# Kernel optimization log

Hardware: AMD Instinct MI355X
Metric: run time of the kernel (lower is better)

The kernel has to match this reference:

```python
import jax, jax.numpy as jnp
import numpy as np

VOL = 100.0  # cubic volume (100,100,100)


def _forward(x, positions, input_weights, features, output_weights,
             connection_radii, thresholds, n_iterations):
    # clamp positions into the volume (per-axis, min 0.1, max VOL-0.1)
    pos = jnp.clip(positions, 0.1, VOL - 0.1)                      # [N,3]
    radii = jnp.clip(connection_radii, 1.0, 50.0)                  # [N]
    # pairwise Euclidean distances via ||a||^2 + ||b||^2 - 2ab (avoids [N,N,3])
    sq = jnp.sum(pos * pos, axis=1)
    d2 = jnp.maximum(sq[:, None] + sq[None, :] - 2.0 * (pos @ pos.T), 0.0)
    pos_mask = d2 > 0.0
    dist = jnp.where(pos_mask, jnp.sqrt(jnp.where(pos_mask, d2, 1.0)), 0.0)  # [N,N]
    max_r = jnp.max(radii)
    conn_mask = (dist < max_r).astype(dist.dtype)
    atten = jnp.exp(-jnp.minimum(dist / (radii[:, None] + 1e-6), 20.0)) * conn_mask
    # feature similarity (F.normalize uses eps as a clamp-min on the norm)
    fn = features / jnp.maximum(jnp.linalg.norm(features, axis=1, keepdims=True), 1e-6)
    feat_sim = fn @ fn.T                                            # [N,N]
    cw = atten * (0.3 + 0.7 * jnp.clip(feat_sim, -1.0, 1.0))
    cw = cw / (jnp.sum(cw, axis=1, keepdims=True) + 1e-6)           # row-normalized [N,N]
    # spatial input / output gating along x-axis
    xc = jnp.clip(pos[:, 0] / VOL, 0.0, 1.0)                        # [N]
    iw = jnp.exp(-3.0 * xc)
    iw = iw / (jnp.sum(iw) + 1e-6)
    act = (x @ input_weights.T) * iw                                # [B,N]
    for _ in range(n_iterations):
        act = jnp.minimum(jax.nn.relu(act + act @ cw.T - thresholds), 100.0)
    ow = jnp.exp(3.0 * (xc - 1.0))
    ow = ow / (jnp.sum(ow) + 1e-6)
    return (act * ow) @ output_weights                              # [B,out]


def setup_inputs() -> dict:
    key = jax.random.key(0)
    ks = jax.random.split(key, 5)
    N, IN, OUT, FD, B = 8000, 784, 10, 32, 64
    return {
        "x": jax.random.normal(ks[0], (B, IN), jnp.float32),
        "positions": jax.random.uniform(ks[1], (N, 3), jnp.float32) * VOL,
        "input_weights": jax.random.normal(ks[2], (N, IN), jnp.float32) * 0.01,
        "features": jax.random.normal(ks[3], (N, FD), jnp.float32) * 0.1,
        "output_weights": jax.random.normal(ks[4], (N, OUT), jnp.float32) * 0.01,
        "connection_radii": jnp.ones((N,), jnp.float32) * 15.0,
        "thresholds": jnp.zeros((N,), jnp.float32),
        "n_iterations": 2,
    }


def reference(x, positions, input_weights, features, output_weights,
              connection_radii, thresholds, n_iterations):
    return _forward(x, positions, input_weights, features, output_weights,
                    connection_radii, thresholds, n_iterations)
```

## Files before the change

kernel.cpp:

```cpp
#include <hip/hip_runtime.h>
#include <hip/hip_bf16.h>
#include <math.h>

#define VOLF 100.0f
#define FD 32
#define OUT_DIM 10
#define MAXN 320
#define MAX_LAUNCH_ITERS 4
#define SRW 2
#define SRB 8
#define OB 128
#define CHUNK 28
#define NCHUNK 7
#define LDP 68
#define PS 8

__global__ __launch_bounds__(256) void k_prext(
    const float* __restrict__ x, const float* __restrict__ positions,
    const float* __restrict__ radii_in, const float* __restrict__ features,
    float* __restrict__ xT, float* __restrict__ posx4,
    float* __restrict__ radii, float* __restrict__ e_iw, float* __restrict__ e_ow,
    float* __restrict__ fn, float* __restrict__ scal, int N, int B, int IN, int nxt)
{
    if ((int)blockIdx.x < nxt) {
        int idx = blockIdx.x * 256 + threadIdx.x;
        if (idx < B * IN) {
            int b = idx / IN, k = idx % IN;
            xT[(size_t)k * B + b] = x[idx];
        }
        return;
    }
    int i = (blockIdx.x - nxt) * 256 + threadIdx.x;
    float my_iw = 0.0f, my_ow = 0.0f, my_r = 0.0f;
    if (i < N) {
        float px = fminf(fmaxf(positions[3*i+0], 0.1f), VOLF - 0.1f);
        float py = fminf(fmaxf(positions[3*i+1], 0.1f), VOLF - 0.1f);
        float pz = fminf(fmaxf(positions[3*i+2], 0.1f), VOLF - 0.1f);
        float sq = px*px + py*py + pz*pz;
        posx4[4*i+0] = px; posx4[4*i+1] = py; posx4[4*i+2] = pz; posx4[4*i+3] = sq;
        float r = fminf(fmaxf(radii_in[i], 1.0f), 50.0f);
        radii[i] = r; my_r = r;
        float xc = fminf(fmaxf(px / VOLF, 0.0f), 1.0f);
        my_iw = expf(-3.0f * xc);
        my_ow = expf(3.0f * (xc - 1.0f));
        e_iw[i] = my_iw; e_ow[i] = my_ow;
        float s = 0.0f;
        #pragma unroll
        for (int k = 0; k < FD; k++) { float v = features[(size_t)i*FD + k]; s += v*v; }
        float nrm = fmaxf(sqrtf(s), 1e-6f);
        #pragma unroll
        for (int k = 0; k < FD; k++) fn[(size_t)i*FD + k] = features[(size_t)i*FD + k] / nrm;
    }
    __shared__ float red[256];
    red[threadIdx.x] = my_iw; __syncthreads();
    for (int s = 128; s > 0; s >>= 1) { if (threadIdx.x < s) red[threadIdx.x] += red[threadIdx.x + s]; __syncthreads(); }
    if (threadIdx.x == 0) atomicAdd(&scal[0], red[0]);
    __syncthreads();
    red[threadIdx.x] = my_ow; __syncthreads();
    for (int s = 128; s > 0; s >>= 1) { if (threadIdx.x < s) red[threadIdx.x] += red[threadIdx.x + s]; __syncthreads(); }
    if (threadIdx.x == 0) atomicAdd(&scal[1], red[0]);
    if (i < N) atomicMax((int*)&scal[2], __float_as_int(my_r));
}

__global__ __launch_bounds__(256) void k_act0(
    const float* __restrict__ xT, const float* __restrict__ Wi,
    float* __restrict__ partial, int N, int IN)
{
    __shared__ float smem[2 * 64 * 68];
    float* wtT = smem;
    int t = threadIdx.x;
    int wave = t >> 6, lane = t & 63;
    int nr = lane >> 2, br = lane & 3;
    int i0 = blockIdx.x * 64;
    int kbase = blockIdx.y * 196;
    float acc[4][16];
    #pragma unroll
    for (int a = 0; a < 4; a++)
        #pragma unroll
        for (int b = 0; b < 16; b++) acc[a][b] = 0.0f;

    for (int c = 0; c < NCHUNK; c++) {
        int k0 = kbase + c * CHUNK;
        __syncthreads();
        for (int fi = t; fi < 64 * (CHUNK/4); fi += 256) {
            int n = fi / (CHUNK/4), q = fi % (CHUNK/4);
            float4 w4 = *(const float4*)(Wi + (size_t)(i0 + n) * IN + k0 + q * 4);
            wtT[(q*4+0)*LDP + n] = w4.x;
            wtT[(q*4+1)*LDP + n] = w4.y;
            wtT[(q*4+2)*LDP + n] = w4.z;
            wtT[(q*4+3)*LDP + n] = w4.w;
        }
        __syncthreads();
        for (int q = ((wave + c) & 3); q < CHUNK/4; q += 4) {
            #pragma unroll
            for (int j = 0; j < 4; j++) {
                int kl = q*4 + j;
                float4 a4 = *(const float4*)(&wtT[kl * LDP + nr*4]);
                const float* xr = xT + (size_t)(k0 + kl) * 64 + br*16;
                float4 b0 = *(const float4*)(xr + 0);
                float4 b1 = *(const float4*)(xr + 4);
                float4 b2 = *(const float4*)(xr + 8);
                float4 b3 = *(const float4*)(xr + 12);
                #pragma unroll
                for (int a = 0; a < 4; a++) {
                    float av = (a==0) ? a4.x : (a==1) ? a4.y : (a==2) ? a4.z : a4.w;
                    acc[a][ 0] += av*b0.x; acc[a][ 1] += av*b0.y; acc[a][ 2] += av*b0.z; acc[a][ 3] += av*b0.w;
                    acc[a][ 4] += av*b1.x; acc[a][ 5] += av*b1.y; acc[a][ 6] += av*b1.z; acc[a][ 7] += av*b1.w;
                    acc[a][ 8] += av*b2.x; acc[a][ 9] += av*b2.y; acc[a][10] += av*b2.z; acc[a][11] += av*b2.w;
                    acc[a][12] += av*b3.x; acc[a][13] += av*b3.y; acc[a][14] += av*b3.z; acc[a][15] += av*b3.w;
                }
            }
        }
    }
    __syncthreads();
    float4* sm4 = (float4*)smem;
    int g = wave >> 1;
    if (wave & 1) {
        #pragma unroll
        for (int a = 0; a < 4; a++)
            #pragma unroll
            for (int b4 = 0; b4 < 4; b4++)
                sm4[(g*16 + a*4 + b4) * 64 + lane] =
                    make_float4(acc[a][b4*4+0], acc[a][b4*4+1], acc[a][b4*4+2], acc[a][b4*4+3]);
    }
    __syncthreads();
    if (!(wave & 1)) {
        int slot = blockIdx.y * 2 + g;
        size_t pbase = ((size_t)slot * N + i0 + nr*4) * 64 + br*16;
        #pragma unroll
        for (int a = 0; a < 4; a++)
            #pragma unroll
            for (int b4 = 0; b4 < 4; b4++) {
                float4 o = sm4[(g*16 + a*4 + b4) * 64 + lane];
                o.x += acc[a][b4*4+0]; o.y += acc[a][b4*4+1];
                o.z += acc[a][b4*4+2]; o.w += acc[a][b4*4+3];
                *(float4*)(partial + pbase + (size_t)a * 64 + b4*4) = o;
            }
    }
}

__global__ __launch_bounds__(256) void k_act0_red(
    const float* __restrict__ partial, const float* __restrict__ e_iw,
    const float* __restrict__ scal, float* __restrict__ actA, int N)
{
    int idx = blockIdx.x * 256 + threadIdx.x;
    int i = idx >> 6;
    size_t stride = (size_t)N * 64;
    float s = 0.0f;
    #pragma unroll
    for (int p = 0; p < PS; p++) s += partial[p * stride + idx];
    float inv = 1.0f / (scal[0] + 1e-6f);
    actA[idx] = s * (e_iw[i] * inv);
}

__device__ __forceinline__ void scan_body(
    const float4& p, const float4& q, int j, float maxr,
    unsigned long long lmask, int2* __restrict__ ep, size_t base, int& cnt)
{
    float d2 = fmaxf(p.w + q.w - 2.0f*(p.x*q.x + p.y*q.y + p.z*q.z), 0.0f);
    float dist = sqrtf(d2);
    bool hit = dist < maxr;
    unsigned long long m = __ballot(hit);
    if (m) {
        if (hit) {
            int pos = cnt + (int)__popcll(m & lmask);
            if (pos < MAXN) ep[base + pos] = make_int2(j, __float_as_int(dist));
        }
        cnt += (int)__popcll(m);
    }
}

__global__ __launch_bounds__(256) void k_scan(
    const float* __restrict__ posx4, const float* __restrict__ scal,
    const float* __restrict__ fn, const float* __restrict__ radii,
    int2* __restrict__ ep, int* __restrict__ nbr_cnt, float* __restrict__ rowinv, int N)
{
    int wave = threadIdx.x >> 6, lane = threadIdx.x & 63;
    int r0 = blockIdx.x * SRB + wave * SRW;
    float4 p0 = ((const float4*)posx4)[r0];
    float4 p1 = ((const float4*)posx4)[r0 + 1];
    float maxr = __int_as_float(((const int*)scal)[2]);
    unsigned long long lmask = (1ull << lane) - 1ull;
    int c0 = 0, c1 = 0;
    size_t base0 = (size_t)r0 * MAXN, base1 = base0 + MAXN;
    int jb = 0;
    for (; jb + 128 <= N; jb += 128) {
        int j0 = jb + lane, j1 = jb + 64 + lane;
        float4 q0 = ((const float4*)posx4)[j0];
        float4 q1 = ((const float4*)posx4)[j1];
        scan_body(p0, q0, j0, maxr, lmask, ep, base0, c0);
        scan_body(p1, q0, j0, maxr, lmask, ep, base1, c1);
        scan_body(p0, q1, j1, maxr, lmask, ep, base0, c0);
        scan_body(p1, q1, j1, maxr, lmask, ep, base1, c1);
    }
    for (; jb < N; jb += 64) {
        int j0 = jb + lane;
        float4 q0 = ((const float4*)posx4)[j0];
        scan_body(p0, q0, j0, maxr, lmask, ep, base0, c0);
        scan_body(p1, q0, j0, maxr, lmask, ep, base1, c1);
    }
    if (lane == 0) {
        nbr_cnt[r0]     = min(c0, MAXN);
        nbr_cnt[r0 + 1] = min(c1, MAXN);
    }
    int sub = lane & 7;
    int eg  = lane >> 3;
    #pragma unroll
    for (int rr = 0; rr < SRW; rr++) {
        int r = r0 + rr;
        int cnt = min(rr == 0 ? c0 : c1, MAXN);
        size_t base = (size_t)r * MAXN;
        float4 fni = ((const float4*)(fn + (size_t)r * FD))[sub];
        float inv_ri = 1.0f / (radii[r] + 1e-6f);
        float s = 0.0f;
        for (int e0 = 0; e0 < cnt; e0 += 8) {
            int e = e0 + eg;
            bool act = e < cnt;
            int ecl = act ? e : cnt - 1;
            int2 edge = ep[base + ecl];
            float dist = __int_as_float(edge.y);
            float4 fj = ((const float4*)(fn + (size_t)edge.x * FD))[sub];
            float fs = fni.x*fj.x + fni.y*fj.y + fni.z*fj.z + fni.w*fj.w;
            fs += __shfl_xor(fs, 1, 64);
            fs += __shfl_xor(fs, 2, 64);
            fs += __shfl_xor(fs, 4, 64);
            fs = fminf(fmaxf(fs, -1.0f), 1.0f);
            float w = expf(-fminf(dist * inv_ri, 20.0f)) * (0.3f + 0.7f * fs);
            if (act && sub == 0) {
                ((float*)&ep[base + e])[1] = w;
                s += w;
            }
        }
        s += __shfl_xor(s, 1, 64);  s += __shfl_xor(s, 2, 64);  s += __shfl_xor(s, 4, 64);
        s += __shfl_xor(s, 8, 64);  s += __shfl_xor(s, 16, 64); s += __shfl_xor(s, 32, 64);
        if (lane == 0) rowinv[r] = 1.0f / (s + 1e-6f);
    }
}

__global__ __launch_bounds__(256) void k_iter(
    const float* __restrict__ actIn, float* __restrict__ actOut,
    const int2* __restrict__ ep, const int* __restrict__ nbr_cnt,
    const float* __restrict__ rowinv, const float* __restrict__ thr,
    const int* __restrict__ nIterPtr, int iterIdx, int N)
{
    if (iterIdx >= min(*nIterPtr, MAX_LAUNCH_ITERS)) return;
    int i = blockIdx.x;
    int wave = threadIdx.x >> 6, lane = threadIdx.x & 63;
    int cnt = nbr_cnt[i];
    float acc = 0.0f;
    for (int e = wave; e < cnt; e += 4) {
        int2 edge = ep[(size_t)i * MAXN + e];
        acc += actIn[(size_t)edge.x * 64 + lane] * __int_as_float(edge.y);
    }
    __shared__ float redA[4 * 64];
    redA[wave * 64 + lane] = acc;
    __syncthreads();
    if (wave == 0) {
        float tot = redA[lane] + redA[64 + lane] + redA[128 + lane] + redA[192 + lane];
        float v = actIn[(size_t)i * 64 + lane] + tot * rowinv[i] - thr[i];
        v = fminf(fmaxf(v, 0.0f), 100.0f);
        actOut[(size_t)i * 64 + lane] = v;
    }
}

__global__ __launch_bounds__(256) void k_out1(
    const float* __restrict__ actA, const float* __restrict__ actB,
    const int* __restrict__ nIterPtr, const float* __restrict__ e_ow,
    const float* __restrict__ scal, const float* __restrict__ outW,
    float* __restrict__ outPart, int N)
{
    int m = min(*nIterPtr, MAX_LAUNCH_ITERS);
    const float* actF = (m & 1) ? actB : actA;
    int wave = threadIdx.x >> 6, lane = threadIdx.x & 63;
    float inv = 1.0f / (scal[1] + 1e-6f);
    float acc[OUT_DIM];
    #pragma unroll
    for (int o = 0; o < OUT_DIM; o++) acc[o] = 0.0f;
    for (int i = blockIdx.x * 4 + wave; i < N; i += OB * 4) {
        float a = actF[(size_t)i * 64 + lane] * (e_ow[i] * inv);
        const float* wo = outW + (size_t)i * OUT_DIM;
        #pragma unroll
        for (int o = 0; o < OUT_DIM; o++) acc[o] += a * wo[o];
    }
    __shared__ float red[4][OUT_DIM][64];
    #pragma unroll
    for (int o = 0; o < OUT_DIM; o++) red[wave][o][lane] = acc[o];
    __syncthreads();
    if (wave == 0) {
        #pragma unroll
        for (int o = 0; o < OUT_DIM; o++) {
            float s = red[0][o][lane] + red[1][o][lane] + red[2][o][lane] + red[3][o][lane];
            outPart[((size_t)blockIdx.x * OUT_DIM + o) * 64 + lane] = s;
        }
    }
}

__global__ __launch_bounds__(256) void k_out2(
    const float* __restrict__ outPart, float* __restrict__ out)
{
    int t = blockIdx.x * 256 + threadIdx.x;
    if (t >= 64 * OUT_DIM) return;
    int b = t / OUT_DIM, o = t % OUT_DIM;
    float s = 0.0f;
    for (int blk = 0; blk < OB; blk++)
        s += outPart[((size_t)blk * OUT_DIM + o) * 64 + b];
    out[t] = s;
}

extern "C" void kernel_launch(void* const* d_in, const int* in_sizes, int n_in,
                              void* d_out, int out_size, void* d_ws, size_t ws_size,
                              hipStream_t stream)
{
    const float* x        = (const float*)d_in[0];
    const float* positions= (const float*)d_in[1];
    const float* Win      = (const float*)d_in[2];
    const float* features = (const float*)d_in[3];
    const float* Wout     = (const float*)d_in[4];
    const float* radii_in = (const float*)d_in[5];
    const float* thr      = (const float*)d_in[6];
    const int*   nIter    = (const int*)  d_in[7];

    const int N  = in_sizes[5];
    const int IN = in_sizes[2] / N;
    const int B  = in_sizes[0] / IN;

    float* ws = (float*)d_ws;
    size_t off = 0;
    auto alloc = [&](size_t nfloats) { size_t cur = off; off += (nfloats + 63) & ~(size_t)63; return cur; };
    float* xT      = ws + alloc((size_t)B * IN);
    float* posx4   = ws + alloc((size_t)N * 4);
    float* radii   = ws + alloc(N);
    float* e_iw    = ws + alloc(N);
    float* e_ow    = ws + alloc(N);
    float* rowinv  = ws + alloc(N);
    float* scal    = ws + alloc(4);
    float* outPart = ws + alloc((size_t)OB * OUT_DIM * 64);
    float* fn      = ws + alloc((size_t)N * FD);
    float* actA    = ws + alloc((size_t)N * 64);
    float* actB    = ws + alloc((size_t)N * 64);
    int2*  ep      = (int2*)(ws + alloc((size_t)N * MAXN * 2));
    int*   nbr_cnt = (int*)(ws + alloc(N));
    float* partial = (float*)ep;

    hipMemsetAsync(scal, 0, 4 * sizeof(float), stream);

    int nxt = (B * IN + 255) / 256;
    int npre = (N + 255) / 256;
    k_prext<<<nxt + npre, 256, 0, stream>>>(x, positions, radii_in, features,
                                            xT, posx4, radii, e_iw, e_ow, fn, scal,
                                            N, B, IN, nxt);
    k_act0<<<dim3(N / 64, 4), 256, 0, stream>>>(xT, Win, partial, N, IN);
    k_act0_red<<<(N * 64) / 256, 256, 0, stream>>>(partial, e_iw, scal, actA, N);
    k_scan<<<N / SRB, 256, 0, stream>>>(posx4, scal, fn, radii, ep, nbr_cnt, rowinv, N);

    float* bufs[2] = {actA, actB};
    for (int it = 0; it < MAX_LAUNCH_ITERS; it++) {
        k_iter<<<N, 256, 0, stream>>>(bufs[it & 1], bufs[(it + 1) & 1],
                                      ep, nbr_cnt, rowinv, thr, nIter, it, N);
    }
    k_out1<<<OB, 256, 0, stream>>>(actA, actB, nIter, e_ow, scal, Wout, outPart, N);
    k_out2<<<3, 256, 0, stream>>>(outPart, (float*)d_out);
}
```

Measured before the change: 269.0 us.

## Bin positions into a 2D spatial grid to prune the all-pairs neighbor scan

Adds a k_binfill kernel that sorts points into a 5x5 grid of x-y cells. k_scan now only visits the cells within the maximum-radius reach of each row pair, instead of testing all N points. The edge-weight and row-sum pass moves into its own per-row k_weight kernel using four waves. The x transpose now goes through a shared-memory tile. Together these cut the O(N^2) distance work and uncoalesced writes, at the cost of two extra launches, a serial per-cell binning pass, and an assumed batch size of 64 in the transpose.

```diff
diff --git a/kernel.cpp b/kernel.cpp
--- a/kernel.cpp
+++ b/kernel.cpp
@@ -7,26 +7,39 @@
 #define OUT_DIM 10
 #define MAXN 320
 #define MAX_LAUNCH_ITERS 4
-#define SRW 2
-#define SRB 8
 #define OB 128
 #define CHUNK 28
 #define NCHUNK 7
 #define LDP 68
 #define PS 8
+#define NCD 5
+#define CELLW 20.0f
+#define NCELL (NCD*NCD)
 
 __global__ __launch_bounds__(256) void k_prext(
     const float* __restrict__ x, const float* __restrict__ positions,
     const float* __restrict__ radii_in, const float* __restrict__ features,
     float* __restrict__ xT, float* __restrict__ posx4,
     float* __restrict__ radii, float* __restrict__ e_iw, float* __restrict__ e_ow,
-    float* __restrict__ fn, float* __restrict__ scal, int N, int B, int IN, int nxt)
-{
+    float* __restrict__ fn, float* __restrict__ scal, int N, int IN, int nxt)
+{
+    __shared__ float tile[64][65];
+    __shared__ float red[256];
     if ((int)blockIdx.x < nxt) {
-        int idx = blockIdx.x * 256 + threadIdx.x;
-        if (idx < B * IN) {
-            int b = idx / IN, k = idx % IN;
-            xT[(size_t)k * B + b] = x[idx];
+        int w = threadIdx.x >> 6, lane = threadIdx.x & 63;
+        int k0 = blockIdx.x * 64;
+        #pragma unroll
+        for (int r = 0; r < 16; r++) {
+            int b = w * 16 + r;
+            int k = k0 + lane;
+            if (k < IN) tile[lane][b] = x[(size_t)b * IN + k];
+        }
+        __syncthreads();
+        #pragma unroll
+        for (int r = 0; r < 16; r++) {
+            int kl = w * 16 + r;
+            int k = k0 + kl;
+            if (k < IN) xT[(size_t)k * 64 + lane] = tile[kl][lane];
         }
         return;
     }
@@ -51,7 +64,6 @@
         #pragma unroll
         for (int k = 0; k < FD; k++) fn[(size_t)i*FD + k] = features[(size_t)i*FD + k] / nrm;
     }
-    __shared__ float red[256];
     red[threadIdx.x] = my_iw; __syncthreads();
     for (int s = 128; s > 0; s >>= 1) { if (threadIdx.x < s) red[threadIdx.x] += red[threadIdx.x + s]; __syncthreads(); }
     if (threadIdx.x == 0) atomicAdd(&scal[0], red[0]);
@@ -60,6 +72,39 @@
     for (int s = 128; s > 0; s >>= 1) { if (threadIdx.x < s) red[threadIdx.x] += red[threadIdx.x + s]; __syncthreads(); }
     if (threadIdx.x == 0) atomicAdd(&scal[1], red[0]);
     if (i < N) atomicMax((int*)&scal[2], __float_as_int(my_r));
+}
+
+__global__ __launch_bounds__(64) void k_binfill(
+    const float* __restrict__ posx4, float4* __restrict__ posb, int* __restrict__ jmap,
+    int* __restrict__ binoff, int* __restrict__ bincnt, int N)
+{
+    int c = blockIdx.x, lane = threadIdx.x;
+    int offs = 0, mine = 0;
+    for (int jb = 0; jb < N; jb += 64) {
+        float4 q = ((const float4*)posx4)[jb + lane];
+        int ix = min(NCD-1, (int)(q.x * (1.0f/CELLW)));
+        int iy = min(NCD-1, (int)(q.y * (1.0f/CELLW)));
+        int cj = ix * NCD + iy;
+        offs += (int)__popcll(__ballot(cj < c));
+        mine += (int)__popcll(__ballot(cj == c));
+    }
+    unsigned long long lmask = (1ull << lane) - 1ull;
+    int w = 0;
+    for (int jb = 0; jb < N; jb += 64) {
+        int j = jb + lane;
+        float4 q = ((const float4*)posx4)[j];
+        int ix = min(NCD-1, (int)(q.x * (1.0f/CELLW)));
+        int iy = min(NCD-1, (int)(q.y * (1.0f/CELLW)));
+        bool hit = (ix * NCD + iy == c);
+        unsigned long long m = __ballot(hit);
+        if (hit) {
+            int pos = offs + w + (int)__popcll(m & lmask);
+            posb[pos] = q;
+            jmap[pos] = j;
+        }
+        w += (int)__popcll(m);
+    }
+    if (lane == 0) { binoff[c] = offs; bincnt[c] = mine; }
 }
 
 __global__ __launch_bounds__(256) void k_act0(
@@ -154,12 +199,12 @@
 }
 
 __device__ __forceinline__ void scan_body(
-    const float4& p, const float4& q, int j, float maxr,
+    const float4& p, const float4& q, int j, float maxr, bool act,
     unsigned long long lmask, int2* __restrict__ ep, size_t base, int& cnt)
 {
     float d2 = fmaxf(p.w + q.w - 2.0f*(p.x*q.x + p.y*q.y + p.z*q.z), 0.0f);
     float dist = sqrtf(d2);
-    bool hit = dist < maxr;
+    bool hit = act && (dist < maxr);
     unsigned long long m = __ballot(hit);
     if (m) {
         if (hit) {
@@ -171,70 +216,79 @@
 }
 
 __global__ __launch_bounds__(256) void k_scan(
-    const float* __restrict__ posx4, const float* __restrict__ scal,
-    const float* __restrict__ fn, const float* __restrict__ radii,
-    int2* __restrict__ ep, int* __restrict__ nbr_cnt, float* __restrict__ rowinv, int N)
+    const float4* __restrict__ posb, const int* __restrict__ jmap,
+    const float* __restrict__ scal, int2* __restrict__ ep, int* __restrict__ nbr_cnt,
+    const int* __restrict__ binoff, const int* __restrict__ bincnt, int N)
 {
     int wave = threadIdx.x >> 6, lane = threadIdx.x & 63;
-    int r0 = blockIdx.x * SRB + wave * SRW;
-    float4 p0 = ((const float4*)posx4)[r0];
-    float4 p1 = ((const float4*)posx4)[r0 + 1];
+    int s0 = (blockIdx.x * 4 + wave) * 2;
+    float4 p0 = posb[s0], p1 = posb[s0 + 1];
+    int r0 = jmap[s0], r1 = jmap[s0 + 1];
     float maxr = __int_as_float(((const int*)scal)[2]);
+    int R = (int)ceilf(maxr * (1.0f/CELLW));
+    int cxa = min(NCD-1, (int)(p0.x * (1.0f/CELLW))), cya = min(NCD-1, (int)(p0.y * (1.0f/CELLW)));
+    int cxb = min(NCD-1, (int)(p1.x * (1.0f/CELLW))), cyb = min(NCD-1, (int)(p1.y * (1.0f/CELLW)));
+    int ix0 = max(0, min(cxa, cxb) - R), ix1 = min(NCD-1, max(cxa, cxb) + R);
+    int iy0 = max(0, min(cya, cyb) - R), iy1 = min(NCD-1, max(cya, cyb) + R);
     unsigned long long lmask = (1ull << lane) - 1ull;
     int c0 = 0, c1 = 0;
-    size_t base0 = (size_t)r0 * MAXN, base1 = base0 + MAXN;
-    int jb = 0;
-    for (; jb + 128 <= N; jb += 128) {
-        int j0 = jb + lane, j1 = jb + 64 + lane;
-        float4 q0 = ((const float4*)posx4)[j0];
-        float4 q1 = ((const float4*)posx4)[j1];
-        scan_body(p0, q0, j0, maxr, lmask, ep, base0, c0);
-        scan_body(p1, q0, j0, maxr, lmask, ep, base1, c1);
-        scan_body(p0, q1, j1, maxr, lmask, ep, base0, c0);
-        scan_body(p1, q1, j1, maxr, lmask, ep, base1, c1);
-    }
-    for (; jb < N; jb += 64) {
-        int j0 = jb + lane;
-        float4 q0 = ((const float4*)posx4)[j0];
-        scan_body(p0, q0, j0, maxr, lmask, ep, base0, c0);
-        scan_body(p1, q0, j0, maxr, lmask, ep, base1, c1);
+    size_t base0 = (size_t)r0 * MAXN, base1 = (size_t)r1 * MAXN;
+    for (int ix = ix0; ix <= ix1; ix++)
+    for (int iy = iy0; iy <= iy1; iy++) {
+        int c = ix * NCD + iy;
+        int bs = binoff[c], cnt = bincnt[c];
+        for (int sb = 0; sb < cnt; sb += 64) {
+            bool act = (sb + lane) < cnt;
+            int s = act ? (bs + sb + lane) : bs;
+            float4 q = posb[s];
+            int j = jmap[s];
+            scan_body(p0, q, j, maxr, act, lmask, ep, base0, c0);
+            scan_body(p1, q, j, maxr, act, lmask, ep, base1, c1);
+        }
     }
     if (lane == 0) {
-        nbr_cnt[r0]     = min(c0, MAXN);
-        nbr_cnt[r0 + 1] = min(c1, MAXN);
-    }
+        nbr_cnt[r0] = min(c0, MAXN);
+        nbr_cnt[r1] = min(c1, MAXN);
+    }
+}
+
+__global__ __launch_bounds__(256) void k_weight(
+    const float* __restrict__ fn, const float* __restrict__ radii,
+    int2* __restrict__ ep ,
+    const int* __restrict__ nbr_cnt, float* __restrict__ rowinv, int N)
+{
+    int i = blockIdx.x;
+    int lane = threadIdx.x & 63;
+    int wave = threadIdx.x >> 6;
     int sub = lane & 7;
     int eg  = lane >> 3;
-    #pragma unroll
-    for (int rr = 0; rr < SRW; rr++) {
-        int r = r0 + rr;
-        int cnt = min(rr == 0 ? c0 : c1, MAXN);
-        size_t base = (size_t)r * MAXN;
-        float4 fni = ((const float4*)(fn + (size_t)r * FD))[sub];
-        float inv_ri = 1.0f / (radii[r] + 1e-6f);
-        float s = 0.0f;
-        for (int e0 = 0; e0 < cnt; e0 += 8) {
-            int e = e0 + eg;
-            bool act = e < cnt;
-            int ecl = act ? e : cnt - 1;
-            int2 edge = ep[base + ecl];
-            float dist = __int_as_float(edge.y);
-            float4 fj = ((const float4*)(fn + (size_t)edge.x * FD))[sub];
-            float fs = fni.x*fj.x + fni.y*fj.y + fni.z*fj.z + fni.w*fj.w;
-            fs += __shfl_xor(fs, 1, 64);
-            fs += __shfl_xor(fs, 2, 64);
-            fs += __shfl_xor(fs, 4, 64);
-            fs = fminf(fmaxf(fs, -1.0f), 1.0f);
-            float w = expf(-fminf(dist * inv_ri, 20.0f)) * (0.3f + 0.7f * fs);
-            if (act && sub == 0) {
-                ((float*)&ep[base + e])[1] = w;
-                s += w;
-            }
-        }
-        s += __shfl_xor(s, 1, 64);  s += __shfl_xor(s, 2, 64);  s += __shfl_xor(s, 4, 64);
-        s += __shfl_xor(s, 8, 64);  s += __shfl_xor(s, 16, 64); s += __shfl_xor(s, 32, 64);
-        if (lane == 0) rowinv[r] = 1.0f / (s + 1e-6f);
-    }
+    float4 fni = ((const float4*)(fn + (size_t)i * FD))[sub];
+    float inv_ri = 1.0f / (radii[i] + 1e-6f);
+    int cnt = nbr_cnt[i];
+    float s = 0.0f;
+    for (int e0 = wave * 8; e0 < cnt; e0 += 32) {
+        int e = e0 + eg;
+        bool act = e < cnt;
+        int ecl = act ? e : (cnt - 1);
+        int2 edge = ep[(size_t)i * MAXN + ecl];
+        int j      = edge.x;
+        float dist = __int_as_float(edge.y);
+        float4 fj = ((const float4*)(fn + (size_t)j * FD))[sub];
+        float fs = fni.x*fj.x + fni.y*fj.y + fni.z*fj.z + fni.w*fj.w;
+        fs += __shfl_xor(fs, 1, 64);
+        fs += __shfl_xor(fs, 2, 64);
+        fs += __shfl_xor(fs, 4, 64);
+        fs = fminf(fmaxf(fs, -1.0f), 1.0f);
+        float w = expf(-fminf(dist * inv_ri, 20.0f)) * (0.3f + 0.7f * fs);
+        if (act && sub == 0) {
+            ((float*)&ep[(size_t)i * MAXN + e])[1] = w;
+            s += w;
+        }
+    }
+    __shared__ float red[256];
+    red[threadIdx.x] = s; __syncthreads();
+    for (int st = 128; st > 0; st >>= 1) { if (threadIdx.x < st) red[threadIdx.x] += red[threadIdx.x + st]; __syncthreads(); }
+    if (threadIdx.x == 0) rowinv[i] = 1.0f / (red[0] + 1e-6f);
 }
 
 __global__ __launch_bounds__(256) void k_iter(
@@ -323,6 +377,7 @@
     const int N  = in_sizes[5];
     const int IN = in_sizes[2] / N;
     const int B  = in_sizes[0] / IN;
+    (void)B;
 
     float* ws = (float*)d_ws;
     size_t off = 0;
@@ -338,20 +393,26 @@
     float* fn      = ws + alloc((size_t)N * FD);
     float* actA    = ws + alloc((size_t)N * 64);
     float* actB    = ws + alloc((size_t)N * 64);
+    float4* posb   = (float4*)(ws + alloc((size_t)N * 4));
+    int*   jmap    = (int*)(ws + alloc(N));
+    int*   binoff  = (int*)(ws + alloc(64));
+    int*   bincnt  = (int*)(ws + alloc(64));
     int2*  ep      = (int2*)(ws + alloc((size_t)N * MAXN * 2));
     int*   nbr_cnt = (int*)(ws + alloc(N));
     float* partial = (float*)ep;
 
     hipMemsetAsync(scal, 0, 4 * sizeof(float), stream);
 
-    int nxt = (B * IN + 255) / 256;
+    int nxt = (IN + 63) / 64;
     int npre = (N + 255) / 256;
     k_prext<<<nxt + npre, 256, 0, stream>>>(x, positions, radii_in, features,
                                             xT, posx4, radii, e_iw, e_ow, fn, scal,
-                                            N, B, IN, nxt);
+                                            N, IN, nxt);
+    k_binfill<<<NCELL, 64, 0, stream>>>(posx4, posb, jmap, binoff, bincnt, N);
     k_act0<<<dim3(N / 64, 4), 256, 0, stream>>>(xT, Win, partial, N, IN);
     k_act0_red<<<(N * 64) / 256, 256, 0, stream>>>(partial, e_iw, scal, actA, N);
-    k_scan<<<N / SRB, 256, 0, stream>>>(posx4, scal, fn, radii, ep, nbr_cnt, rowinv, N);
+    k_scan<<<N / 8, 256, 0, stream>>>(posb, jmap, scal, ep, nbr_cnt, binoff, bincnt, N);
+    k_weight<<<N, 256, 0, stream>>>(fn, radii, ep, nbr_cnt, rowinv, N);
 
     float* bufs[2] = {actA, actB};
     for (int it = 0; it < MAX_LAUNCH_ITERS; it++) {
```

Measured after the change: 311.0 us. 15.7% more time.
